# Performance work log

Measured on AMD Instinct MI355X. Metric: run time of the kernel, lower is better.

The kernel has to match this reference:

```python
import jax, jax.numpy as jnp
import numpy as np

B, S, DIM, H = 2, 2048, 1024, 16
DK = DIM // H  # 64
NEG = -10000000000.0


def setup_inputs() -> dict:
    key = jax.random.key(0)
    k1, k2, k3, k4, k5, k6 = jax.random.split(key, 6)
    dec_xs = jax.random.normal(k1, (B, S, DIM), dtype=jnp.float32)
    enc_xs = jax.random.normal(k2, (B, S, DIM), dtype=jnp.float32)
    mask = jax.random.randint(k3, (B, S, S), 0, 2, dtype=jnp.int32)
    # torch Linear weights: out = x @ W.T, bias=False
    sc = 1.0 / np.sqrt(DIM)
    Wq = jax.random.normal(k4, (DIM, DIM), dtype=jnp.float32) * sc
    Wkv = jax.random.normal(k5, (2 * DIM, DIM), dtype=jnp.float32) * sc
    Wo = jax.random.normal(k6, (DIM, DIM), dtype=jnp.float32) * sc
    return {"dec_xs": dec_xs, "enc_xs": enc_xs, "Wq": Wq, "Wkv": Wkv, "Wo": Wo, "mask": mask}


def reference(dec_xs, enc_xs, Wq, Wkv, Wo, mask):
    b, s, dim = enc_xs.shape
    qs = dec_xs @ Wq.T                      # [b,s,dim]  (dropout inactive in eval)
    kv = enc_xs @ Wkv.T                     # [b,s,2*dim]
    ks, vs = jnp.split(kv, 2, axis=-1)
    # head layout: view(b, s, dk, h) -- heads LAST, as in the original
    qs = qs.reshape(b, s, DK, H)
    ks = ks.reshape(b, s, DK, H)
    vs = vs.reshape(b, s, DK, H)
    scores = jnp.einsum('bqdh,bkdh->bqkh', qs, ks) / np.sqrt(DK)
    scores = jnp.where(mask[..., None] == 0, NEG, scores)
    weights = jax.nn.softmax(scores, axis=-2)  # softmax over key axis
    out = jnp.einsum('bqkh,bkdh->bqdh', weights, vs).reshape(b, s, dim)
    return out @ Wo.T
```

## Files before the change

kernel.cpp:

```cpp
#include <hip/hip_runtime.h>
#include <hip/hip_bf16.h>

#define BB 2
#define SS 2048
#define DIMM 1024
#define HH 16
#define DKK 64
#define QSCALE 0.18033688011112042592f

using bf16 = __hip_bfloat16;
typedef __attribute__((ext_vector_type(8))) short v8s;
typedef __attribute__((ext_vector_type(4))) short v4s;
typedef __attribute__((ext_vector_type(4))) float f32x4;

__device__ __forceinline__ void cvt4(const float* __restrict__ s,
                                     bf16* __restrict__ d, int idx) {
  const float4 f = ((const float4*)s)[idx];
  bf16 t[4] = {__float2bfloat16(f.x), __float2bfloat16(f.y),
               __float2bfloat16(f.z), __float2bfloat16(f.w)};
  *(v4s*)(d + (size_t)idx * 4) = *(const v4s*)t;
}

__global__ __launch_bounds__(256) void convert_pack_kernel(
    const float* __restrict__ dec, const float* __restrict__ enc,
    const float* __restrict__ Wq, const float* __restrict__ Wkv,
    const float* __restrict__ Wo, const int* __restrict__ mask,
    bf16* __restrict__ decb, bf16* __restrict__ encb, bf16* __restrict__ Wqb,
    bf16* __restrict__ Wkvb, bf16* __restrict__ Wob,
    unsigned long long* __restrict__ mp) {
  const int gid = blockIdx.x * 256 + threadIdx.x;
  const int NT = 256 * 1024;
#pragma unroll
  for (int i = 0; i < 4; ++i) cvt4(dec, decb, gid + i * NT);
#pragma unroll
  for (int i = 0; i < 4; ++i) cvt4(enc, encb, gid + i * NT);
  cvt4(Wq, Wqb, gid);
#pragma unroll
  for (int i = 0; i < 2; ++i) cvt4(Wkv, Wkvb, gid + i * NT);
  cvt4(Wo, Wob, gid);
  const int lane = threadIdx.x & 63;
  const int wave_id = gid >> 6;
  for (int i = 0; i < 32; ++i) {
    const size_t w = (size_t)wave_id * 32 + i;
    const unsigned long long bm = __ballot(mask[w * 64 + lane] != 0);
    if (lane == 0) mp[w] = bm;
  }
}

__global__ __launch_bounds__(256) void proj_gemm_kernel(
    const bf16* __restrict__ decb, const bf16* __restrict__ encb,
    const bf16* __restrict__ Wqb, const bf16* __restrict__ Wkvb,
    bf16* __restrict__ Qr, bf16* __restrict__ Kr, bf16* __restrict__ Vt) {
  __shared__ __align__(16) bf16 As[128][72];
  __shared__ __align__(16) bf16 Bs[128][72];
  const int t = threadIdx.x;
  const int wave = t >> 6, lane = t & 63;
  const int quad = lane >> 4, l15 = lane & 15;
  const int wm = (wave >> 1) * 64, wn = (wave & 1) * 64;
  const int bx = blockIdx.x;
  const int kind = bx >> 3;
  const int g = bx & 7;
  const int m0 = blockIdx.y * 128;

  const bf16* Asrc = (kind == 0) ? decb : encb;
  const bf16* Wsrc = (kind == 0) ? Wqb : Wkvb;

  const int sr = t >> 2;
  const int sc = (t & 3) * 16;
  const int wr0 = sr * 16 + g * 2 + ((kind == 2) ? DIMM : 0);
  const int wr1 = sr * 16 + g * 2 + 1 + ((kind == 2) ? DIMM : 0);

  v8s apf[4], bpf[4];
  auto loadA = [&](int kc) {
    const bf16* p0 = Asrc + (size_t)(m0 + sr) * DIMM + kc + sc;
    apf[0] = ((const v8s*)p0)[0];
    apf[1] = ((const v8s*)p0)[1];
    const bf16* p1 = Asrc + (size_t)(m0 + sr + 64) * DIMM + kc + sc;
    apf[2] = ((const v8s*)p1)[0];
    apf[3] = ((const v8s*)p1)[1];
  };
  auto loadB = [&](int kc) {
    const bf16* q0 = Wsrc + (size_t)wr0 * DIMM + kc + sc;
    bpf[0] = ((const v8s*)q0)[0];
    bpf[1] = ((const v8s*)q0)[1];
    const bf16* q1 = Wsrc + (size_t)wr1 * DIMM + kc + sc;
    bpf[2] = ((const v8s*)q1)[0];
    bpf[3] = ((const v8s*)q1)[1];
  };

  f32x4 acc[4][4] = {};
  loadA(0);
  loadB(0);

  for (int kc = 0; kc < DIMM; kc += 64) {
    __syncthreads();
    *(v8s*)&As[sr][sc] = apf[0];
    *(v8s*)&As[sr][sc + 8] = apf[1];
    *(v8s*)&As[sr + 64][sc] = apf[2];
    *(v8s*)&As[sr + 64][sc + 8] = apf[3];
    *(v8s*)&Bs[sr][sc] = bpf[0];
    *(v8s*)&Bs[sr][sc + 8] = bpf[1];
    *(v8s*)&Bs[sr + 64][sc] = bpf[2];
    *(v8s*)&Bs[sr + 64][sc + 8] = bpf[3];
    if (kc + 64 < DIMM) {
      loadA(kc + 64);
      loadB(kc + 64);
    }
    __syncthreads();
#pragma unroll
    for (int ks = 0; ks < 2; ++ks) {
      v8s af[4], bfr[4];
#pragma unroll
      for (int i = 0; i < 4; ++i)
        af[i] = *(const v8s*)&As[wm + i * 16 + l15][ks * 32 + quad * 8];
#pragma unroll
      for (int j = 0; j < 4; ++j)
        bfr[j] = *(const v8s*)&Bs[wn + j * 16 + l15][ks * 32 + quad * 8];
#pragma unroll
      for (int i = 0; i < 4; ++i)
#pragma unroll
        for (int j = 0; j < 4; ++j)
          acc[i][j] = __builtin_amdgcn_mfma_f32_16x16x32_bf16(
              af[i], bfr[j], acc[i][j], 0, 0, 0);
    }
  }

#pragma unroll
  for (int i = 0; i < 4; ++i) {
#pragma unroll
    for (int r = 0; r < 4; ++r) {
      const int m = m0 + wm + i * 16 + quad * 4 + r;
#pragma unroll
      for (int j = 0; j < 4; ++j) {
        const int c = wn + j * 16 + l15;
        const int np = g * 128 + c;
        const float v = acc[i][j][r];
        if (kind == 0) {
          Qr[(size_t)m * DIMM + np] = __float2bfloat16(v * QSCALE);
        } else if (kind == 1) {
          Kr[(size_t)m * DIMM + np] = __float2bfloat16(v);
        } else {
          const int h = np >> 6, d = np & 63;
          const int b = m >> 11, s = m & (SS - 1);
          Vt[(((size_t)b * HH + h) * DKK + d) * SS + s] = __float2bfloat16(v);
        }
      }
    }
  }
}

__global__ __launch_bounds__(256) void out_gemm_kernel(
    const bf16* __restrict__ A, const bf16* __restrict__ W,
    float* __restrict__ out) {
  __shared__ __align__(16) bf16 As[128][72];
  __shared__ __align__(16) bf16 Bs[64][72];
  const int t = threadIdx.x;
  const int wave = t >> 6, lane = t & 63;
  const int quad = lane >> 4, l15 = lane & 15;
  const int wm = (wave >> 1) * 64, wn = (wave & 1) * 32;
  const int n0 = blockIdx.x * 64;
  const int m0 = blockIdx.y * 128;
  const int sr = t >> 2;
  const int sc = (t & 3) * 16;

  v8s ar[4], br[2];
  auto loadA = [&](int kc) {
#pragma unroll
    for (int rr = 0; rr < 2; ++rr) {
      const bf16* p = A + (size_t)(m0 + sr + rr * 64) * DIMM + kc + sc;
#pragma unroll
      for (int i = 0; i < 2; ++i) ar[rr * 2 + i] = ((const v8s*)p)[i];
    }
  };
  auto loadB = [&](int kc) {
    const bf16* p = W + (size_t)(n0 + sr) * DIMM + kc + sc;
#pragma unroll
    for (int i = 0; i < 2; ++i) br[i] = ((const v8s*)p)[i];
  };

  f32x4 acc[4][2] = {};
  loadA(0);
  loadB(0);
  for (int kc = 0; kc < DIMM; kc += 64) {
    __syncthreads();
#pragma unroll
    for (int rr = 0; rr < 2; ++rr) {
      *(v8s*)&As[sr + rr * 64][sc] = ar[rr * 2 + 0];
      *(v8s*)&As[sr + rr * 64][sc + 8] = ar[rr * 2 + 1];
    }
    *(v8s*)&Bs[sr][sc] = br[0];
    *(v8s*)&Bs[sr][sc + 8] = br[1];
    if (kc + 64 < DIMM) {
      loadA(kc + 64);
      loadB(kc + 64);
    }
    __syncthreads();
#pragma unroll
    for (int ks = 0; ks < 2; ++ks) {
      v8s af[4], bfr[2];
#pragma unroll
      for (int i = 0; i < 4; ++i)
        af[i] = *(const v8s*)&As[wm + i * 16 + l15][ks * 32 + quad * 8];
#pragma unroll
      for (int j = 0; j < 2; ++j)
        bfr[j] = *(const v8s*)&Bs[wn + j * 16 + l15][ks * 32 + quad * 8];
#pragma unroll
      for (int i = 0; i < 4; ++i)
#pragma unroll
        for (int j = 0; j < 2; ++j)
          acc[i][j] = __builtin_amdgcn_mfma_f32_16x16x32_bf16(
              af[i], bfr[j], acc[i][j], 0, 0, 0);
    }
  }

#pragma unroll
  for (int i = 0; i < 4; ++i) {
#pragma unroll
    for (int r = 0; r < 4; ++r) {
      const int m = m0 + wm + i * 16 + quad * 4 + r;
#pragma unroll
      for (int j = 0; j < 2; ++j) {
        const int n = n0 + wn + j * 16 + l15;
        out[(size_t)m * DIMM + n] = acc[i][j][r];
      }
    }
  }
}

__global__ __launch_bounds__(256) void attn_kernel(
    const bf16* __restrict__ Qr, const bf16* __restrict__ Kr,
    const bf16* __restrict__ Vt, const unsigned long long* __restrict__ mp,
    bf16* __restrict__ Ar) {
  __shared__ __align__(16) bf16 Ks[64][72];
  __shared__ __align__(16) bf16 Vs[64][72];
  __shared__ __align__(16) bf16 Ps[4][16][72];

  const int t = threadIdx.x;
  const int wave = t >> 6, lane = t & 63;
  const int quad = lane >> 4, l15 = lane & 15;

  const int bx = blockIdx.x;
  const int xcd = bx & 7, j = bx >> 3;
  const int g = (xcd << 2) | (j & 3);
  const int tile = j >> 2;
  const int h = g & 15, b = g >> 4;

  const int qw = tile * 64 + wave * 16;
  const size_t bhv = ((size_t)b * HH + h) * DKK;

  const bf16* qrow = Qr + ((size_t)(b * SS + qw + l15)) * DIMM + h * 64;
  const v8s aq0 = *(const v8s*)(qrow + quad * 8);
  const v8s aq1 = *(const v8s*)(qrow + 32 + quad * 8);

  f32x4 o[4] = {};
  float lsum[4] = {0.f, 0.f, 0.f, 0.f};

  const int id0 = t * 8;
  const int r0 = id0 >> 6, c0 = id0 & 63;

  for (int kt = 0; kt < 32; ++kt) {
    const int k0 = kt * 64;
    __syncthreads();
    {
      const bf16* kb = Kr + ((size_t)(b * SS + k0 + r0)) * DIMM + h * 64 + c0;
      *(v8s*)&Ks[r0][c0] = *(const v8s*)kb;
      *(v8s*)&Ks[r0 + 32][c0] = *(const v8s*)(kb + (size_t)32 * DIMM);
      *(v8s*)&Vs[r0][c0] = *(const v8s*)(Vt + (bhv + r0) * SS + k0 + c0);
      *(v8s*)&Vs[r0 + 32][c0] =
          *(const v8s*)(Vt + (bhv + r0 + 32) * SS + k0 + c0);
    }
    __syncthreads();

    unsigned long long mw[4];
#pragma unroll
    for (int r = 0; r < 4; ++r)
      mw[r] = mp[((size_t)b * SS + qw + quad * 4 + r) * 32 + kt] >> l15;

    f32x4 sc[4];
#pragma unroll
    for (int n = 0; n < 4; ++n) {
      const v8s bk0 = *(const v8s*)&Ks[n * 16 + l15][quad * 8];
      const v8s bk1 = *(const v8s*)&Ks[n * 16 + l15][32 + quad * 8];
      f32x4 z = {0.f, 0.f, 0.f, 0.f};
      z = __builtin_amdgcn_mfma_f32_16x16x32_bf16(aq0, bk0, z, 0, 0, 0);
      sc[n] = __builtin_amdgcn_mfma_f32_16x16x32_bf16(aq1, bk1, z, 0, 0, 0);
    }

#pragma unroll
    for (int n = 0; n < 4; ++n)
#pragma unroll
      for (int r = 0; r < 4; ++r) {
        const bool keep = (mw[r] >> (n * 16)) & 1ULL;
        const float p = keep ? __builtin_amdgcn_exp2f(sc[n][r]) : 0.f;
        sc[n][r] = p;
        lsum[r] += p;
      }

#pragma unroll
    for (int n = 0; n < 4; ++n)
#pragma unroll
      for (int r = 0; r < 4; ++r)
        Ps[wave][quad * 4 + r][n * 16 + l15] = __float2bfloat16(sc[n][r]);
    const v8s ap0 = *(const v8s*)&Ps[wave][l15][quad * 8];
    const v8s ap1 = *(const v8s*)&Ps[wave][l15][32 + quad * 8];

#pragma unroll
    for (int n = 0; n < 4; ++n) {
      const v8s bv0 = *(const v8s*)&Vs[n * 16 + l15][quad * 8];
      const v8s bv1 = *(const v8s*)&Vs[n * 16 + l15][32 + quad * 8];
      o[n] = __builtin_amdgcn_mfma_f32_16x16x32_bf16(ap0, bv0, o[n], 0, 0, 0);
      o[n] = __builtin_amdgcn_mfma_f32_16x16x32_bf16(ap1, bv1, o[n], 0, 0, 0);
    }
  }

#pragma unroll
  for (int r = 0; r < 4; ++r) {
    float l = lsum[r];
    l += __shfl_xor(l, 1);
    l += __shfl_xor(l, 2);
    l += __shfl_xor(l, 4);
    l += __shfl_xor(l, 8);
    const float inv = 1.f / l;
    const size_t row = (size_t)b * SS + qw + quad * 4 + r;
#pragma unroll
    for (int n = 0; n < 4; ++n) {
      const int d = n * 16 + l15;
      Ar[row * DIMM + d * 16 + h] = __float2bfloat16(o[n][r] * inv);
    }
  }
}

extern "C" void kernel_launch(void* const* d_in, const int* in_sizes, int n_in,
                              void* d_out, int out_size, void* d_ws,
                              size_t ws_size, hipStream_t stream) {
  const float* dec = (const float*)d_in[0];
  const float* enc = (const float*)d_in[1];
  const float* Wq = (const float*)d_in[2];
  const float* Wkv = (const float*)d_in[3];
  const float* Wo = (const float*)d_in[4];
  const int* mask = (const int*)d_in[5];
  float* out = (float*)d_out;

  bf16* decb = (bf16*)d_out;
  bf16* Wqb = (bf16*)((char*)d_out + ((size_t)2 * SS * DIMM * 2));

  char* ws = (char*)d_ws;
  size_t off = 0;
  bf16* encb = (bf16*)(ws + off);
  bf16* Ar = (bf16*)(ws + off);   off += (size_t)2 * SS * DIMM * 2;
  bf16* Wkvb = (bf16*)(ws + off); off += (size_t)2 * DIMM * DIMM * 2;
  bf16* Wob = (bf16*)(ws + off);  off += (size_t)DIMM * DIMM * 2;
  bf16* Qr = (bf16*)(ws + off);   off += (size_t)2 * SS * DIMM * 2;
  bf16* Kr = (bf16*)(ws + off);   off += (size_t)2 * SS * DIMM * 2;
  bf16* Vt = (bf16*)(ws + off);   off += (size_t)2 * SS * DIMM * 2;
  unsigned long long* mp = (unsigned long long*)(ws + off);

  dim3 blk(256);
  convert_pack_kernel<<<dim3(1024), blk, 0, stream>>>(
      dec, enc, Wq, Wkv, Wo, mask, decb, encb, Wqb, Wkvb, Wob, mp);
  proj_gemm_kernel<<<dim3(24, 32), blk, 0, stream>>>(decb, encb, Wqb, Wkvb, Qr,
                                                     Kr, Vt);
  attn_kernel<<<dim3(1024), blk, 0, stream>>>(Qr, Kr, Vt, mp, Ar);
  out_gemm_kernel<<<dim3(16, 32), blk, 0, stream>>>(Ar, Wob, out);
}
```

Before: 286.8 us.

## Process two 64-row query sub-tiles per attention block to reuse K/V tiles

Each attention block now handles 128 query rows (two 64-row sub-tiles per wave set) instead of 64, so every K/V tile loaded into shared memory and into registers is used twice. The grid is halved to 512 blocks. This cuts global K/V traffic and LDS fragment reads per query row, at the cost of more registers per thread (two sets of accumulators, Q fragments and cached K/V fragments) and fewer blocks to fill the GPU.

```diff
diff --git a/kernel.cpp b/kernel.cpp
--- a/kernel.cpp
+++ b/kernel.cpp
@@ -245,15 +245,21 @@
   const int tile = j >> 2;
   const int h = g & 15, b = g >> 4;
 
-  const int qw = tile * 64 + wave * 16;
+  const int qb = tile * 128;
   const size_t bhv = ((size_t)b * HH + h) * DKK;
 
-  const bf16* qrow = Qr + ((size_t)(b * SS + qw + l15)) * DIMM + h * 64;
-  const v8s aq0 = *(const v8s*)(qrow + quad * 8);
-  const v8s aq1 = *(const v8s*)(qrow + 32 + quad * 8);
-
-  f32x4 o[4] = {};
-  float lsum[4] = {0.f, 0.f, 0.f, 0.f};
+  v8s aq[2][2];
+#pragma unroll
+  for (int qs = 0; qs < 2; ++qs) {
+    const bf16* qrow =
+        Qr + ((size_t)(b * SS + qb + qs * 64 + wave * 16 + l15)) * DIMM +
+        h * 64;
+    aq[qs][0] = *(const v8s*)(qrow + quad * 8);
+    aq[qs][1] = *(const v8s*)(qrow + 32 + quad * 8);
+  }
+
+  f32x4 o[2][4] = {};
+  float lsum[2][4] = {};
 
   const int id0 = t * 8;
   const int r0 = id0 >> 6, c0 = id0 & 63;
@@ -271,63 +277,79 @@
     }
     __syncthreads();
 
-    unsigned long long mw[4];
-#pragma unroll
-    for (int r = 0; r < 4; ++r)
-      mw[r] = mp[((size_t)b * SS + qw + quad * 4 + r) * 32 + kt] >> l15;
-
-    f32x4 sc[4];
+    v8s bk[4][2], bv[4][2];
 #pragma unroll
     for (int n = 0; n < 4; ++n) {
-      const v8s bk0 = *(const v8s*)&Ks[n * 16 + l15][quad * 8];
-      const v8s bk1 = *(const v8s*)&Ks[n * 16 + l15][32 + quad * 8];
-      f32x4 z = {0.f, 0.f, 0.f, 0.f};
-      z = __builtin_amdgcn_mfma_f32_16x16x32_bf16(aq0, bk0, z, 0, 0, 0);
-      sc[n] = __builtin_amdgcn_mfma_f32_16x16x32_bf16(aq1, bk1, z, 0, 0, 0);
-    }
-
-#pragma unroll
-    for (int n = 0; n < 4; ++n)
-#pragma unroll
-      for (int r = 0; r < 4; ++r) {
-        const bool keep = (mw[r] >> (n * 16)) & 1ULL;
-        const float p = keep ? __builtin_amdgcn_exp2f(sc[n][r]) : 0.f;
-        sc[n][r] = p;
-        lsum[r] += p;
-      }
-
-#pragma unroll
-    for (int n = 0; n < 4; ++n)
+      bk[n][0] = *(const v8s*)&Ks[n * 16 + l15][quad * 8];
+      bk[n][1] = *(const v8s*)&Ks[n * 16 + l15][32 + quad * 8];
+      bv[n][0] = *(const v8s*)&Vs[n * 16 + l15][quad * 8];
+      bv[n][1] = *(const v8s*)&Vs[n * 16 + l15][32 + quad * 8];
+    }
+
+#pragma unroll
+    for (int qs = 0; qs < 2; ++qs) {
+      const int qw = qb + qs * 64 + wave * 16;
+      unsigned long long mw[4];
 #pragma unroll
       for (int r = 0; r < 4; ++r)
-        Ps[wave][quad * 4 + r][n * 16 + l15] = __float2bfloat16(sc[n][r]);
-    const v8s ap0 = *(const v8s*)&Ps[wave][l15][quad * 8];
-    const v8s ap1 = *(const v8s*)&Ps[wave][l15][32 + quad * 8];
-
-#pragma unroll
-    for (int n = 0; n < 4; ++n) {
-      const v8s bv0 = *(const v8s*)&Vs[n * 16 + l15][quad * 8];
-      const v8s bv1 = *(const v8s*)&Vs[n * 16 + l15][32 + quad * 8];
-      o[n] = __builtin_amdgcn_mfma_f32_16x16x32_bf16(ap0, bv0, o[n], 0, 0, 0);
-      o[n] = __builtin_amdgcn_mfma_f32_16x16x32_bf16(ap1, bv1, o[n], 0, 0, 0);
-    }
-  }
-
-#pragma unroll
-  for (int r = 0; r < 4; ++r) {
-    float l = lsum[r];
-    l += __shfl_xor(l, 1);
-    l += __shfl_xor(l, 2);
-    l += __shfl_xor(l, 4);
-    l += __shfl_xor(l, 8);
-    const float inv = 1.f / l;
-    const size_t row = (size_t)b * SS + qw + quad * 4 + r;
-#pragma unroll
-    for (int n = 0; n < 4; ++n) {
-      const int d = n * 16 + l15;
-      Ar[row * DIMM + d * 16 + h] = __float2bfloat16(o[n][r] * inv);
-    }
-  }
+        mw[r] = mp[((size_t)b * SS + qw + quad * 4 + r) * 32 + kt] >> l15;
+
+      f32x4 sc[4];
+#pragma unroll
+      for (int n = 0; n < 4; ++n) {
+        f32x4 z = {0.f, 0.f, 0.f, 0.f};
+        z = __builtin_amdgcn_mfma_f32_16x16x32_bf16(aq[qs][0], bk[n][0], z, 0,
+                                                    0, 0);
+        sc[n] = __builtin_amdgcn_mfma_f32_16x16x32_bf16(aq[qs][1], bk[n][1], z,
+                                                        0, 0, 0);
+      }
+
+#pragma unroll
+      for (int n = 0; n < 4; ++n)
+#pragma unroll
+        for (int r = 0; r < 4; ++r) {
+          const bool keep = (mw[r] >> (n * 16)) & 1ULL;
+          const float p = keep ? __builtin_amdgcn_exp2f(sc[n][r]) : 0.f;
+          sc[n][r] = p;
+          lsum[qs][r] += p;
+        }
+
+#pragma unroll
+      for (int n = 0; n < 4; ++n)
+#pragma unroll
+        for (int r = 0; r < 4; ++r)
+          Ps[wave][quad * 4 + r][n * 16 + l15] = __float2bfloat16(sc[n][r]);
+      const v8s ap0 = *(const v8s*)&Ps[wave][l15][quad * 8];
+      const v8s ap1 = *(const v8s*)&Ps[wave][l15][32 + quad * 8];
+
+#pragma unroll
+      for (int n = 0; n < 4; ++n) {
+        o[qs][n] = __builtin_amdgcn_mfma_f32_16x16x32_bf16(ap0, bv[n][0],
+                                                           o[qs][n], 0, 0, 0);
+        o[qs][n] = __builtin_amdgcn_mfma_f32_16x16x32_bf16(ap1, bv[n][1],
+                                                           o[qs][n], 0, 0, 0);
+      }
+    }
+  }
+
+#pragma unroll
+  for (int qs = 0; qs < 2; ++qs)
+#pragma unroll
+    for (int r = 0; r < 4; ++r) {
+      float l = lsum[qs][r];
+      l += __shfl_xor(l, 1);
+      l += __shfl_xor(l, 2);
+      l += __shfl_xor(l, 4);
+      l += __shfl_xor(l, 8);
+      const float inv = 1.f / l;
+      const size_t row =
+          (size_t)b * SS + qb + qs * 64 + wave * 16 + quad * 4 + r;
+#pragma unroll
+      for (int n = 0; n < 4; ++n) {
+        const int d = n * 16 + l15;
+        Ar[row * DIMM + d * 16 + h] = __float2bfloat16(o[qs][n][r] * inv);
+      }
+    }
 }
 
 extern "C" void kernel_launch(void* const* d_in, const int* in_sizes, int n_in,
@@ -360,6 +382,6 @@
       dec, enc, Wq, Wkv, Wo, mask, decb, encb, Wqb, Wkvb, Wob, mp);
   proj_gemm_kernel<<<dim3(24, 32), blk, 0, stream>>>(decb, encb, Wqb, Wkvb, Qr,
                                                      Kr, Vt);
-  attn_kernel<<<dim3(1024), blk, 0, stream>>>(Qr, Kr, Vt, mp, Ar);
+  attn_kernel<<<dim3(512), blk, 0, stream>>>(Qr, Kr, Vt, mp, Ar);
   out_gemm_kernel<<<dim3(16, 32), blk, 0, stream>>>(Ar, Wob, out);
 }
```

Result: no change. 287.5 us (+0.2%).
